# Kernel optimization log

Measured on AMD Instinct MI355X. Metric: run time of the kernel, lower is better.

The kernel has to match this reference:

```python
import jax, jax.numpy as jnp
import numpy as np

DIM = 512
HEADS = 8
DIM_HEAD = 64
INNER = HEADS * DIM_HEAD
SCALE = DIM_HEAD ** -0.5
EPS = 1e-5


def setup_inputs() -> dict:
    key = jax.random.key(0)
    ks = jax.random.split(key, 7)
    B, N = 8, 1024
    x = jax.random.normal(ks[0], (B, N, DIM), dtype=jnp.float32)
    ORquery = jax.random.normal(ks[1], (B, N, DIM), dtype=jnp.float32)
    alpha = jax.random.uniform(ks[2], (B, N, N), dtype=jnp.float32)
    # learned params (Linear layers without bias; stored as [in, out])
    w_qkv = jax.random.normal(ks[3], (DIM, INNER * 3), dtype=jnp.float32) * (DIM ** -0.5)
    w_orq = jax.random.normal(ks[4], (DIM, INNER), dtype=jnp.float32) * (DIM ** -0.5)
    w_out = jax.random.normal(ks[5], (INNER, DIM), dtype=jnp.float32) * (INNER ** -0.5)
    ln_w = jnp.ones((DIM,), dtype=jnp.float32)
    ln_b = jnp.zeros((DIM,), dtype=jnp.float32)
    return {"x": x, "ORquery": ORquery, "alpha": alpha, "ln_w": ln_w,
            "ln_b": ln_b, "w_qkv": w_qkv, "w_orq": w_orq, "w_out": w_out}


def _layernorm(x, w, b):
    mu = jnp.mean(x, axis=-1, keepdims=True)
    var = jnp.mean(jnp.square(x - mu), axis=-1, keepdims=True)
    return (x - mu) * jax.lax.rsqrt(var + EPS) * w + b


def _split_heads(t):  # [B, N, H*D] -> [B, H, N, D]
    B, N, _ = t.shape
    return t.reshape(B, N, HEADS, DIM_HEAD).transpose(0, 2, 1, 3)


def _merge_heads(t):  # [B, H, N, D] -> [B, N, H*D]
    B, H, N, D = t.shape
    return t.transpose(0, 2, 1, 3).reshape(B, N, H * D)


def reference(x, ORquery, alpha, ln_w, ln_b, w_qkv, w_orq, w_out):
    xn = _layernorm(x, ln_w, ln_b)
    qkv = xn @ w_qkv  # [B, N, 3*INNER]
    q, k, v = jnp.split(qkv, 3, axis=-1)
    q, k, v = _split_heads(q), _split_heads(k), _split_heads(v)

    # standard attention pass
    dots = jnp.einsum('bhid,bhjd->bhij', q, k) * SCALE
    attn = jax.nn.softmax(dots, axis=-1)
    out = _merge_heads(jnp.einsum('bhij,bhjd->bhid', attn, v))

    # OR-query pass: shared K/V, diagonal logits zeroed, (1-alpha^T) rescale
    orq = _split_heads(_layernorm(ORquery, ln_w, ln_b) @ w_orq)
    ordots = jnp.einsum('bhid,bhjd->bhij', orq, k) * SCALE
    N = ordots.shape[-1]
    eye = jnp.eye(N, dtype=bool)
    ordots = jnp.where(eye, 0.0, ordots)
    ordots = ordots * (1.0 - alpha.transpose(0, 2, 1)[:, None, :, :])
    orattn = jax.nn.softmax(ordots, axis=-1)
    orout = _merge_heads(jnp.einsum('bhij,bhjd->bhid', orattn, v))

    return (out @ w_out, orout @ w_out)
```

## Files before the change

kernel.cpp:

```cpp
#include <hip/hip_runtime.h>
#include <hip/hip_fp16.h>
#include <cstdint>
#include <cstddef>

typedef unsigned short u16;
typedef unsigned int u32;
typedef __attribute__((ext_vector_type(8))) short short8;
typedef __attribute__((ext_vector_type(4))) float f32x4;

static __device__ __forceinline__ u16 f2bf(float x) {
    u32 u = __builtin_bit_cast(u32, x);
    u += 0x7FFFu + ((u >> 16) & 1u);
    return (u16)(u >> 16);
}

static __device__ __forceinline__ void gload16(const void* g, void* l) {
    __builtin_amdgcn_global_load_lds(
        (const __attribute__((address_space(1))) u32*)g,
        (__attribute__((address_space(3))) u32*)l, 16, 0, 0);
}

#define SW(row, cb) (((row) * 64) + ((((cb) ^ ((row) & 7))) * 8))

#define C_L2E 0.18033688011112042f

static __device__ __forceinline__ void wtrans_body(
    const float* __restrict__ src, u16* __restrict__ dst, int R, int C,
    int bx, int by, float t[32][33])
{
    int c0 = bx * 32, r0 = by * 32;
    int tx = threadIdx.x & 31, ty = threadIdx.x >> 5;
    #pragma unroll
    for (int rr = 0; rr < 32; rr += 8)
        t[ty + rr][tx] = src[(size_t)(r0 + ty + rr) * C + c0 + tx];
    __syncthreads();
    #pragma unroll
    for (int rr = 0; rr < 32; rr += 8)
        dst[(size_t)(c0 + ty + rr) * R + r0 + tx] = f2bf(t[tx][ty + rr]);
}

__global__ __launch_bounds__(256) void prep_kernel(
    const float* __restrict__ x, const float* __restrict__ orqy,
    const float* __restrict__ alpha,
    const float* __restrict__ lw, const float* __restrict__ lb,
    const float* __restrict__ w_qkv, const float* __restrict__ w_orq,
    const float* __restrict__ w_out,
    u16* __restrict__ xn, u16* __restrict__ orqn,
    u16* __restrict__ wqkvT, u16* __restrict__ worqT, u16* __restrict__ woutT,
    u16* __restrict__ ascT)
{
    __shared__ float t[32][33];
    int id = blockIdx.x;
    if (id < 768) {
        wtrans_body(w_qkv, wqkvT, 512, 1536, id % 48, id / 48, t);
    } else if (id < 1024) {
        int r = id - 768;
        wtrans_body(w_orq, worqT, 512, 512, r & 15, r >> 4, t);
    } else if (id < 1280) {
        int r = id - 1024;
        wtrans_body(w_out, woutT, 512, 512, r & 15, r >> 4, t);
    } else if (id < 9472) {
        int r = id - 1280;
        int bx = r & 31, by = (r >> 5) & 31, b = r >> 10;
        int i0 = by * 32, j0 = bx * 32;
        int tx = threadIdx.x & 31, ty = threadIdx.x >> 5;
        const float* ab = alpha + ((size_t)b << 20);
        u16* atb = ascT + ((size_t)b << 20);
        #pragma unroll
        for (int rr = 0; rr < 32; rr += 8)
            t[ty + rr][tx] = ab[(size_t)(j0 + ty + rr) * 1024 + i0 + tx];
        __syncthreads();
        #pragma unroll
        for (int rr = 0; rr < 32; rr += 8) {
            float v = C_L2E * (1.0f - t[tx][ty + rr]);
            __half hv = __float2half_rn(v);
            atb[(size_t)(i0 + ty + rr) * 1024 + j0 + tx] = __builtin_bit_cast(u16, hv);
        }
    } else {
        int row = (id - 9472) * 4 + (threadIdx.x >> 6);
        const float* src;
        u16* dst;
        if (row < 8192) { src = x + (size_t)row * 512; dst = xn + (size_t)row * 512; }
        else { src = orqy + (size_t)(row - 8192) * 512; dst = orqn + (size_t)(row - 8192) * 512; }
        int lane = threadIdx.x & 63;
        float4 a = *(const float4*)(src + lane * 8);
        float4 b = *(const float4*)(src + lane * 8 + 4);
        float s = a.x + a.y + a.z + a.w + b.x + b.y + b.z + b.w;
        float q = a.x*a.x + a.y*a.y + a.z*a.z + a.w*a.w
                + b.x*b.x + b.y*b.y + b.z*b.z + b.w*b.w;
        #pragma unroll
        for (int off = 32; off >= 1; off >>= 1) {
            s += __shfl_xor(s, off);
            q += __shfl_xor(q, off);
        }
        float mu = s * (1.0f / 512.0f);
        float var = q * (1.0f / 512.0f) - mu * mu;
        float rs = 1.0f / sqrtf(var + 1e-5f);
        float4 w0 = *(const float4*)(lw + lane * 8);
        float4 w1 = *(const float4*)(lw + lane * 8 + 4);
        float4 b0 = *(const float4*)(lb + lane * 8);
        float4 b1 = *(const float4*)(lb + lane * 8 + 4);
        union { u16 h[8]; uint4 v; } ou;
        ou.h[0] = f2bf((a.x - mu) * rs * w0.x + b0.x);
        ou.h[1] = f2bf((a.y - mu) * rs * w0.y + b0.y);
        ou.h[2] = f2bf((a.z - mu) * rs * w0.z + b0.z);
        ou.h[3] = f2bf((a.w - mu) * rs * w0.w + b0.w);
        ou.h[4] = f2bf((b.x - mu) * rs * w1.x + b1.x);
        ou.h[5] = f2bf((b.y - mu) * rs * w1.y + b1.y);
        ou.h[6] = f2bf((b.z - mu) * rs * w1.z + b1.z);
        ou.h[7] = f2bf((b.w - mu) * rs * w1.w + b1.w);
        *(uint4*)(dst + lane * 8) = ou.v;
    }
}

__global__ __launch_bounds__(256) void gemm_kernel(
    const u16* __restrict__ A_, const u16* __restrict__ Bt_,
    const u16* __restrict__ A2, const u16* __restrict__ Bt2,
    int N, int K, int mode,
    u16* __restrict__ oq, u16* __restrict__ ok, u16* __restrict__ ov,
    u16* __restrict__ oq2, float* __restrict__ of)
{
    __shared__ u16 As[8192];
    __shared__ u16 Bs[8192];
    int bx = blockIdx.x;
    const u16* A = A_;
    const u16* Bt = Bt_;
    bool orqblk = false;
    if (mode == 3 && bx >= 12) { A = A2; Bt = Bt2; orqblk = true; bx -= 12; }
    int m0 = blockIdx.y * 128, n0 = bx * 128;
    int tid = threadIdx.x;
    int w = tid >> 6, lane = tid & 63;
    int lo = lane & 15, hi = lane >> 4;
    int wm = (w >> 1) * 64, wn = (w & 1) * 64;

    int sr0 = tid >> 2, sr1 = sr0 + 64;
    int sc0 = ((tid & 3) ^ ((sr0 >> 1) & 3)) * 8;
    int sc1 = ((tid & 3) ^ ((sr1 >> 1) & 3)) * 8;
    const u16* aS0 = A + (size_t)(m0 + sr0) * K + sc0;
    const u16* aS1 = A + (size_t)(m0 + sr1) * K + sc1;
    const u16* bS0 = Bt + (size_t)(n0 + sr0) * K + sc0;
    const u16* bS1 = Bt + (size_t)(n0 + sr1) * K + sc1;
    int d0 = w * 512, d1 = 2048 + w * 512;

    int aoff[4], boff[4];
    #pragma unroll
    for (int f = 0; f < 4; ++f) {
        int ra = wm + f * 16 + lo, rb = wn + f * 16 + lo;
        aoff[f] = ra * 32 + ((hi ^ ((ra >> 1) & 3)) * 8);
        boff[f] = rb * 32 + ((hi ^ ((rb >> 1) & 3)) * 8);
    }

    f32x4 acc[4][4] = {};
    int nk = K >> 5;
    gload16(aS0, &As[d0]);
    gload16(aS1, &As[d1]);
    gload16(bS0, &Bs[d0]);
    gload16(bS1, &Bs[d1]);
    __syncthreads();
    for (int kt = 0; kt < nk; ++kt) {
        int cur = (kt & 1) << 12;
        if (kt + 1 < nk) {
            int ko = (kt + 1) * 32;
            int nxt = ((kt + 1) & 1) << 12;
            gload16(aS0 + ko, &As[nxt + d0]);
            gload16(aS1 + ko, &As[nxt + d1]);
            gload16(bS0 + ko, &Bs[nxt + d0]);
            gload16(bS1 + ko, &Bs[nxt + d1]);
        }
        short8 af[4], bfr[4];
        #pragma unroll
        for (int mf = 0; mf < 4; ++mf) af[mf] = *(const short8*)&As[cur + aoff[mf]];
        #pragma unroll
        for (int nf = 0; nf < 4; ++nf) bfr[nf] = *(const short8*)&Bs[cur + boff[nf]];
        #pragma unroll
        for (int mf = 0; mf < 4; ++mf)
            #pragma unroll
            for (int nf = 0; nf < 4; ++nf)
                acc[mf][nf] = __builtin_amdgcn_mfma_f32_16x16x32_bf16(af[mf], bfr[nf], acc[mf][nf], 0, 0, 0);
        __syncthreads();
    }
    #pragma unroll
    for (int mf = 0; mf < 4; ++mf) {
        #pragma unroll
        for (int nf = 0; nf < 4; ++nf) {
            #pragma unroll
            for (int r = 0; r < 4; ++r) {
                int row = m0 + wm + mf * 16 + hi * 4 + r;
                int col = n0 + wn + nf * 16 + lo;
                float val = acc[mf][nf][r];
                if (mode == 2) {
                    of[(size_t)row * N + col] = val;
                } else {
                    int bb = row >> 10, i = row & 1023;
                    int h = (col >> 6) & 7;
                    int d = col & 63;
                    if (orqblk) {
                        oq2[(((size_t)bb * 8 + h) * 1024 + i) * 64 + d] = f2bf(val);
                    } else {
                        int which = col >> 9;
                        if (which == 0) val *= C_L2E;
                        u16 bv = f2bf(val);
                        if (which == 2) {
                            ov[(((size_t)bb * 8 + h) * 64 + d) * 1024 + i] = bv;
                        } else {
                            size_t idx = (((size_t)bb * 8 + h) * 1024 + i) * 64 + d;
                            (which == 0 ? oq : ok)[idx] = bv;
                        }
                    }
                }
            }
        }
    }
}

__global__ __launch_bounds__(512) void attn_fused_kernel(
    const u16* __restrict__ Q, const u16* __restrict__ OQ,
    const u16* __restrict__ Kk, const u16* __restrict__ Vt,
    const u16* __restrict__ asc,
    u16* __restrict__ outS, u16* __restrict__ outO)
{
    __shared__ u16 Kbuf[2][8192];
    __shared__ u16 Vbuf[2][8192];
    __shared__ u16 Ps[8192];

    int id = blockIdx.x;
    int swz = (id & 7) * 64 + (id >> 3);
    int bh = swz >> 3, it = swz & 7;
    int b = bh >> 3, h = bh & 7;
    int i0 = it * 128;
    int tid = threadIdx.x;
    int w = tid >> 6, lane = tid & 63;
    int lo = lane & 15, hi = lane >> 4;

    const u16* Qb = Q + ((size_t)bh * 1024 + i0) * 64;
    const u16* Ob = OQ + ((size_t)bh * 1024 + i0) * 64;
    const u16* Kb = Kk + (size_t)bh * 1024 * 64;
    const u16* Vb = Vt + (size_t)bh * 64 * 1024;

    int sxc = ((lane & 7) ^ (lane >> 3)) * 8;
    int krow0 = w * 16 + (lane >> 3);
    const u16* kS = Kb + (size_t)krow0 * 64 + sxc;
    int vrow = w * 8 + (lane >> 3);
    int sxv = ((lane & 7) ^ (vrow & 7)) * 8;
    const u16* vS = Vb + (size_t)vrow * 1024 + sxv;
    int kd = w * 1024;
    int vd = w * 512;

    const u16* AbL = asc + ((size_t)b << 20) + ((size_t)(i0 + w * 16 + hi * 4) << 10) + lo;

    int qrow = w * 16 + lo;
    short8 qS0 = *(const short8*)&Qb[qrow * 64 + hi * 8];
    short8 qS1 = *(const short8*)&Qb[qrow * 64 + 32 + hi * 8];
    short8 qO0 = *(const short8*)&Ob[qrow * 64 + hi * 8];
    short8 qO1 = *(const short8*)&Ob[qrow * 64 + 32 + hi * 8];

    int jtd = it * 2 + (w >> 2);

    gload16(kS, &Kbuf[0][kd]);
    gload16(kS + 512, &Kbuf[0][kd + 512]);
    gload16(vS, &Vbuf[0][vd]);
    gload16(vS + 64, &Vbuf[0][vd + 4096]);
    __syncthreads();

    f32x4 oS[4] = {}, oO[4] = {};
    float mS[4], lS[4], mO[4], lO[4];
    #pragma unroll
    for (int r = 0; r < 4; ++r) { mS[r] = -1e30f; lS[r] = 0.f; mO[r] = -1e30f; lO[r] = 0.f; }

    for (int jt = 0; jt < 8; ++jt) {
        int j0 = jt * 128;
        int c = jt & 1;

        u16 a_[32];
        #pragma unroll
        for (int sub = 0; sub < 2; ++sub)
            #pragma unroll
            for (int jf = 0; jf < 4; ++jf)
                #pragma unroll
                for (int r = 0; r < 4; ++r)
                    a_[sub * 16 + jf * 4 + r] = AbL[(size_t)(r << 10) + j0 + sub * 64 + jf * 16];

        if (jt < 7) {
            int jn = j0 + 128;
            gload16(kS + (size_t)jn * 64, &Kbuf[c ^ 1][kd]);
            gload16(kS + (size_t)(jn + 8) * 64, &Kbuf[c ^ 1][kd + 512]);
            gload16(vS + jn, &Vbuf[c ^ 1][vd]);
            gload16(vS + jn + 64, &Vbuf[c ^ 1][vd + 4096]);
        }

        #pragma unroll
        for (int sub = 0; sub < 2; ++sub) {
            const u16* Kc = &Kbuf[c][sub * 4096];
            const u16* Vc = &Vbuf[c][sub * 4096];
            const u16* al = &a_[sub * 16];

            f32x4 s[4];
            #pragma unroll
            for (int jf = 0; jf < 4; ++jf) {
                short8 kf0 = *(const short8*)&Kc[SW(jf * 16 + lo, hi)];
                short8 kf1 = *(const short8*)&Kc[SW(jf * 16 + lo, 4 + hi)];
                f32x4 z = {};
                z = __builtin_amdgcn_mfma_f32_16x16x32_bf16(qS0, kf0, z, 0, 0, 0);
                z = __builtin_amdgcn_mfma_f32_16x16x32_bf16(qS1, kf1, z, 0, 0, 0);
                s[jf] = z;
            }
            {
                float mx4[4];
                #pragma unroll
                for (int r = 0; r < 4; ++r)
                    mx4[r] = fmaxf(fmaxf(s[0][r], s[1][r]), fmaxf(s[2][r], s[3][r]));
                float need = fmaxf(fmaxf(mx4[0] - mS[0], mx4[1] - mS[1]),
                                   fmaxf(mx4[2] - mS[2], mx4[3] - mS[3]));
                if (!__all(need <= 8.0f)) {
                    #pragma unroll
                    for (int r = 0; r < 4; ++r) {
                        float mx = mx4[r];
                        #pragma unroll
                        for (int msk = 8; msk >= 1; msk >>= 1) mx = fmaxf(mx, __shfl_xor(mx, msk));
                        float mn = fmaxf(mS[r], mx);
                        float scl = __builtin_amdgcn_exp2f(mS[r] - mn);
                        mS[r] = mn;
                        lS[r] *= scl;
                        #pragma unroll
                        for (int df = 0; df < 4; ++df) oS[df][r] *= scl;
                    }
                }
                #pragma unroll
                for (int r = 0; r < 4; ++r)
                    #pragma unroll
                    for (int jf = 0; jf < 4; ++jf) {
                        float p = __builtin_amdgcn_exp2f(s[jf][r] - mS[r]);
                        s[jf][r] = p;
                        lS[r] += p;
                    }
            }
            #pragma unroll
            for (int jf = 0; jf < 4; ++jf)
                #pragma unroll
                for (int r = 0; r < 4; r += 2) {
                    int p0 = hi * 4 + r, p1 = p0 + 1;
                    u32 pk;
                    asm("v_cvt_pk_bf16_f32 %0, %1, %2" : "=v"(pk) : "v"(s[jf][r]), "v"(s[jf][r + 1]));
                    Ps[w * 1024 + p0 * 64 + ((jf * 16 + lo) ^ ((p0 & 7) * 8))] = (u16)pk;
                    Ps[w * 1024 + p1 * 64 + ((jf * 16 + lo) ^ ((p1 & 7) * 8))] = (u16)(pk >> 16);
                }
            {
                short8 pa0 = *(const short8*)&Ps[w * 1024 + SW(lo, hi)];
                short8 pa1 = *(const short8*)&Ps[w * 1024 + SW(lo, 4 + hi)];
                #pragma unroll
                for (int df = 0; df < 4; ++df) {
                    short8 v0 = *(const short8*)&Vc[SW(df * 16 + lo, hi)];
                    short8 v1 = *(const short8*)&Vc[SW(df * 16 + lo, 4 + hi)];
                    oS[df] = __builtin_amdgcn_mfma_f32_16x16x32_bf16(pa0, v0, oS[df], 0, 0, 0);
                    oS[df] = __builtin_amdgcn_mfma_f32_16x16x32_bf16(pa1, v1, oS[df], 0, 0, 0);
                }
            }

            #pragma unroll
            for (int jf = 0; jf < 4; ++jf) {
                short8 kf0 = *(const short8*)&Kc[SW(jf * 16 + lo, hi)];
                short8 kf1 = *(const short8*)&Kc[SW(jf * 16 + lo, 4 + hi)];
                f32x4 z = {};
                z = __builtin_amdgcn_mfma_f32_16x16x32_bf16(qO0, kf0, z, 0, 0, 0);
                z = __builtin_amdgcn_mfma_f32_16x16x32_bf16(qO1, kf1, z, 0, 0, 0);
                s[jf] = z;
            }
            #pragma unroll
            for (int jf = 0; jf < 4; ++jf)
                #pragma unroll
                for (int r = 0; r < 4; ++r) {
                    __half hv = __builtin_bit_cast(__half, al[jf * 4 + r]);
                    s[jf][r] *= __half2float(hv);
                }
            if (jt * 2 + sub == jtd) {
                #pragma unroll
                for (int jf = 0; jf < 4; ++jf)
                    #pragma unroll
                    for (int r = 0; r < 4; ++r)
                        s[jf][r] = ((jf == (w & 3)) && (hi * 4 + r == lo)) ? 0.0f : s[jf][r];
            }
            {
                float mx4[4];
                #pragma unroll
                for (int r = 0; r < 4; ++r)
                    mx4[r] = fmaxf(fmaxf(s[0][r], s[1][r]), fmaxf(s[2][r], s[3][r]));
                float need = fmaxf(fmaxf(mx4[0] - mO[0], mx4[1] - mO[1]),
                                   fmaxf(mx4[2] - mO[2], mx4[3] - mO[3]));
                if (!__all(need <= 8.0f)) {
                    #pragma unroll
                    for (int r = 0; r < 4; ++r) {
                        float mx = mx4[r];
                        #pragma unroll
                        for (int msk = 8; msk >= 1; msk >>= 1) mx = fmaxf(mx, __shfl_xor(mx, msk));
                        float mn = fmaxf(mO[r], mx);
                        float scl = __builtin_amdgcn_exp2f(mO[r] - mn);
                        mO[r] = mn;
                        lO[r] *= scl;
                        #pragma unroll
                        for (int df = 0; df < 4; ++df) oO[df][r] *= scl;
                    }
                }
                #pragma unroll
                for (int r = 0; r < 4; ++r)
                    #pragma unroll
                    for (int jf = 0; jf < 4; ++jf) {
                        float p = __builtin_amdgcn_exp2f(s[jf][r] - mO[r]);
                        s[jf][r] = p;
                        lO[r] += p;
                    }
            }
            #pragma unroll
            for (int jf = 0; jf < 4; ++jf)
                #pragma unroll
                for (int r = 0; r < 4; r += 2) {
                    int p0 = hi * 4 + r, p1 = p0 + 1;
                    u32 pk;
                    asm("v_cvt_pk_bf16_f32 %0, %1, %2" : "=v"(pk) : "v"(s[jf][r]), "v"(s[jf][r + 1]));
                    Ps[w * 1024 + p0 * 64 + ((jf * 16 + lo) ^ ((p0 & 7) * 8))] = (u16)pk;
                    Ps[w * 1024 + p1 * 64 + ((jf * 16 + lo) ^ ((p1 & 7) * 8))] = (u16)(pk >> 16);
                }
            {
                short8 pa0 = *(const short8*)&Ps[w * 1024 + SW(lo, hi)];
                short8 pa1 = *(const short8*)&Ps[w * 1024 + SW(lo, 4 + hi)];
                #pragma unroll
                for (int df = 0; df < 4; ++df) {
                    short8 v0 = *(const short8*)&Vc[SW(df * 16 + lo, hi)];
                    short8 v1 = *(const short8*)&Vc[SW(df * 16 + lo, 4 + hi)];
                    oO[df] = __builtin_amdgcn_mfma_f32_16x16x32_bf16(pa0, v0, oO[df], 0, 0, 0);
                    oO[df] = __builtin_amdgcn_mfma_f32_16x16x32_bf16(pa1, v1, oO[df], 0, 0, 0);
                }
            }
        }

        __syncthreads();
    }

    #pragma unroll
    for (int r = 0; r < 4; ++r) {
        float a = lS[r], c2 = lO[r];
        #pragma unroll
        for (int msk = 8; msk >= 1; msk >>= 1) {
            a += __shfl_xor(a, msk);
            c2 += __shfl_xor(c2, msk);
        }
        lS[r] = 1.0f / a;
        lO[r] = 1.0f / c2;
    }
    size_t obase = ((size_t)b * 1024 + i0 + w * 16 + hi * 4) * 512 + h * 64 + lo;
    #pragma unroll
    for (int df = 0; df < 4; ++df)
        #pragma unroll
        for (int r = 0; r < 4; ++r) {
            outS[obase + (size_t)r * 512 + df * 16] = f2bf(oS[df][r] * lS[r]);
            outO[obase + (size_t)r * 512 + df * 16] = f2bf(oO[df][r] * lO[r]);
        }
}

extern "C" void kernel_launch(void* const* d_in, const int* in_sizes, int n_in,
                              void* d_out, int out_size, void* d_ws, size_t ws_size,
                              hipStream_t stream)
{
    const float* x     = (const float*)d_in[0];
    const float* orqy  = (const float*)d_in[1];
    const float* alpha = (const float*)d_in[2];
    const float* ln_w  = (const float*)d_in[3];
    const float* ln_b  = (const float*)d_in[4];
    const float* w_qkv = (const float*)d_in[5];
    const float* w_orq = (const float*)d_in[6];
    const float* w_out = (const float*)d_in[7];
    float* outp = (float*)d_out;

    char* base = (char*)d_ws;
    size_t off = 0;
    auto alloc = [&](size_t bytes) -> char* {
        char* r = base + off;
        off += (bytes + 255) & ~(size_t)255;
        return r;
    };
    const size_t RC = 8192ull * 512 * 2;
    u16* xn       = (u16*)alloc(RC);
    u16* orqn     = (u16*)alloc(RC);
    u16* qb       = (u16*)alloc(RC);
    u16* kb       = (u16*)alloc(RC);
    u16* vb       = (u16*)alloc(RC);
    u16* orqb     = (u16*)alloc(RC);
    u16* attout   = (u16*)alloc(RC);
    u16* orattout = (u16*)alloc(RC);
    u16* wqkvT    = (u16*)alloc(1536ull * 512 * 2);
    u16* worqT    = (u16*)alloc(512ull * 512 * 2);
    u16* woutT    = (u16*)alloc(512ull * 512 * 2);
    u16* ascT     = (u16*)alloc(8ull * 1024 * 1024 * 2);

    prep_kernel<<<13568, 256, 0, stream>>>(x, orqy, alpha, ln_w, ln_b,
                                           w_qkv, w_orq, w_out,
                                           xn, orqn, wqkvT, worqT, woutT, ascT);
    gemm_kernel<<<dim3(16, 64), 256, 0, stream>>>(xn, wqkvT, orqn, worqT,
                                                  1536, 512, 3,
                                                  qb, kb, vb, orqb, nullptr);
    attn_fused_kernel<<<dim3(512), 512, 0, stream>>>(qb, orqb, kb, vb, ascT, attout, orattout);
    gemm_kernel<<<dim3(4, 128), 256, 0, stream>>>(attout, woutT, nullptr, nullptr,
                                                  512, 512, 2,
                                                  nullptr, nullptr, nullptr, nullptr, outp);
}
```

Baseline: 163.1 us.

## Overlap alpha and w_out transposes with GEMM/attention and enlarge GEMM tiles

After: 166.0 us. No clear change (+1.8%).

```diff
diff --git a/kernel.cpp b/kernel.cpp
--- a/kernel.cpp
+++ b/kernel.cpp
@@ -29,7 +29,7 @@
     int bx, int by, float t[32][33])
 {
     int c0 = bx * 32, r0 = by * 32;
-    int tx = threadIdx.x & 31, ty = threadIdx.x >> 5;
+    int tx = threadIdx.x & 31, ty = (threadIdx.x & 255) >> 5;
     #pragma unroll
     for (int rr = 0; rr < 32; rr += 8)
         t[ty + rr][tx] = src[(size_t)(r0 + ty + rr) * C + c0 + tx];
@@ -41,13 +41,10 @@
 
 __global__ __launch_bounds__(256) void prep_kernel(
     const float* __restrict__ x, const float* __restrict__ orqy,
-    const float* __restrict__ alpha,
     const float* __restrict__ lw, const float* __restrict__ lb,
     const float* __restrict__ w_qkv, const float* __restrict__ w_orq,
-    const float* __restrict__ w_out,
     u16* __restrict__ xn, u16* __restrict__ orqn,
-    u16* __restrict__ wqkvT, u16* __restrict__ worqT, u16* __restrict__ woutT,
-    u16* __restrict__ ascT)
+    u16* __restrict__ wqkvT, u16* __restrict__ worqT)
 {
     __shared__ float t[32][33];
     int id = blockIdx.x;
@@ -56,28 +53,8 @@
     } else if (id < 1024) {
         int r = id - 768;
         wtrans_body(w_orq, worqT, 512, 512, r & 15, r >> 4, t);
-    } else if (id < 1280) {
-        int r = id - 1024;
-        wtrans_body(w_out, woutT, 512, 512, r & 15, r >> 4, t);
-    } else if (id < 9472) {
-        int r = id - 1280;
-        int bx = r & 31, by = (r >> 5) & 31, b = r >> 10;
-        int i0 = by * 32, j0 = bx * 32;
-        int tx = threadIdx.x & 31, ty = threadIdx.x >> 5;
-        const float* ab = alpha + ((size_t)b << 20);
-        u16* atb = ascT + ((size_t)b << 20);
-        #pragma unroll
-        for (int rr = 0; rr < 32; rr += 8)
-            t[ty + rr][tx] = ab[(size_t)(j0 + ty + rr) * 1024 + i0 + tx];
-        __syncthreads();
-        #pragma unroll
-        for (int rr = 0; rr < 32; rr += 8) {
-            float v = C_L2E * (1.0f - t[tx][ty + rr]);
-            __half hv = __float2half_rn(v);
-            atb[(size_t)(i0 + ty + rr) * 1024 + j0 + tx] = __builtin_bit_cast(u16, hv);
-        }
     } else {
-        int row = (id - 9472) * 4 + (threadIdx.x >> 6);
+        int row = (id - 1024) * 4 + (threadIdx.x >> 6);
         const float* src;
         u16* dst;
         if (row < 8192) { src = x + (size_t)row * 512; dst = xn + (size_t)row * 512; }
@@ -113,34 +90,64 @@
     }
 }
 
-__global__ __launch_bounds__(256) void gemm_kernel(
+__global__ __launch_bounds__(512) void gemm_kernel(
     const u16* __restrict__ A_, const u16* __restrict__ Bt_,
     const u16* __restrict__ A2, const u16* __restrict__ Bt2,
+    const float* __restrict__ alpha, u16* __restrict__ ascT,
     int N, int K, int mode,
     u16* __restrict__ oq, u16* __restrict__ ok, u16* __restrict__ ov,
     u16* __restrict__ oq2, float* __restrict__ of)
 {
-    __shared__ u16 As[8192];
+    __shared__ u16 As[16384];
     __shared__ u16 Bs[8192];
+    int tid = threadIdx.x;
+
+    if (mode == 3 && blockIdx.y >= 32) {
+        float (*t)[32][33] = (float(*)[32][33])As;
+        int aid = blockIdx.x + (blockIdx.y - 32) * 16;
+        int sub = tid >> 8;
+        int t2 = tid & 255;
+        int tx = t2 & 31, ty = t2 >> 5;
+        for (int it2 = 0; it2 < 16; ++it2) {
+            int g = aid * 32 + it2 * 2 + sub;
+            int b = g >> 10, rr_ = g & 1023;
+            int i0 = (rr_ >> 5) * 32, j0 = (rr_ & 31) * 32;
+            const float* ab = alpha + ((size_t)b << 20);
+            u16* atb = ascT + ((size_t)b << 20);
+            #pragma unroll
+            for (int rr = 0; rr < 32; rr += 8)
+                t[sub][ty + rr][tx] = ab[(size_t)(j0 + ty + rr) * 1024 + i0 + tx];
+            __syncthreads();
+            #pragma unroll
+            for (int rr = 0; rr < 32; rr += 8) {
+                float v = C_L2E * (1.0f - t[sub][tx][ty + rr]);
+                __half hv = __float2half_rn(v);
+                atb[(size_t)(i0 + ty + rr) * 1024 + j0 + tx] = __builtin_bit_cast(u16, hv);
+            }
+            __syncthreads();
+        }
+        return;
+    }
+
     int bx = blockIdx.x;
     const u16* A = A_;
     const u16* Bt = Bt_;
     bool orqblk = false;
     if (mode == 3 && bx >= 12) { A = A2; Bt = Bt2; orqblk = true; bx -= 12; }
-    int m0 = blockIdx.y * 128, n0 = bx * 128;
-    int tid = threadIdx.x;
+    int m0 = blockIdx.y * 256, n0 = bx * 128;
     int w = tid >> 6, lane = tid & 63;
     int lo = lane & 15, hi = lane >> 4;
     int wm = (w >> 1) * 64, wn = (w & 1) * 64;
 
-    int sr0 = tid >> 2, sr1 = sr0 + 64;
-    int sc0 = ((tid & 3) ^ ((sr0 >> 1) & 3)) * 8;
-    int sc1 = ((tid & 3) ^ ((sr1 >> 1) & 3)) * 8;
-    const u16* aS0 = A + (size_t)(m0 + sr0) * K + sc0;
-    const u16* aS1 = A + (size_t)(m0 + sr1) * K + sc1;
-    const u16* bS0 = Bt + (size_t)(n0 + sr0) * K + sc0;
-    const u16* bS1 = Bt + (size_t)(n0 + sr1) * K + sc1;
-    int d0 = w * 512, d1 = 2048 + w * 512;
+    int arow0 = w * 32 + (lane >> 2);
+    int brow  = w * 16 + (lane >> 2);
+    int acb0 = ((lane & 3) ^ ((arow0 >> 1) & 3)) * 8;
+    int acb1 = ((lane & 3) ^ (((arow0 + 16) >> 1) & 3)) * 8;
+    int bcb  = ((lane & 3) ^ ((brow >> 1) & 3)) * 8;
+    const u16* aS0 = A + (size_t)(m0 + arow0) * K + acb0;
+    const u16* aS1 = A + (size_t)(m0 + arow0 + 16) * K + acb1;
+    const u16* bS0 = Bt + (size_t)(n0 + brow) * K + bcb;
+    int dA0 = w * 1024, dA1 = w * 1024 + 512, dB = w * 512;
 
     int aoff[4], boff[4];
     #pragma unroll
@@ -152,26 +159,26 @@
 
     f32x4 acc[4][4] = {};
     int nk = K >> 5;
-    gload16(aS0, &As[d0]);
-    gload16(aS1, &As[d1]);
-    gload16(bS0, &Bs[d0]);
-    gload16(bS1, &Bs[d1]);
+    gload16(aS0, &As[dA0]);
+    gload16(aS1, &As[dA1]);
+    gload16(bS0, &Bs[dB]);
     __syncthreads();
     for (int kt = 0; kt < nk; ++kt) {
-        int cur = (kt & 1) << 12;
+        int curA = (kt & 1) << 13;
+        int curB = (kt & 1) << 12;
         if (kt + 1 < nk) {
             int ko = (kt + 1) * 32;
-            int nxt = ((kt + 1) & 1) << 12;
-            gload16(aS0 + ko, &As[nxt + d0]);
-            gload16(aS1 + ko, &As[nxt + d1]);
-            gload16(bS0 + ko, &Bs[nxt + d0]);
-            gload16(bS1 + ko, &Bs[nxt + d1]);
+            int nxA = ((kt + 1) & 1) << 13;
+            int nxB = ((kt + 1) & 1) << 12;
+            gload16(aS0 + ko, &As[nxA + dA0]);
+            gload16(aS1 + ko, &As[nxA + dA1]);
+            gload16(bS0 + ko, &Bs[nxB + dB]);
         }
         short8 af[4], bfr[4];
         #pragma unroll
-        for (int mf = 0; mf < 4; ++mf) af[mf] = *(const short8*)&As[cur + aoff[mf]];
-        #pragma unroll
-        for (int nf = 0; nf < 4; ++nf) bfr[nf] = *(const short8*)&Bs[cur + boff[nf]];
+        for (int mf = 0; mf < 4; ++mf) af[mf] = *(const short8*)&As[curA + aoff[mf]];
+        #pragma unroll
+        for (int nf = 0; nf < 4; ++nf) bfr[nf] = *(const short8*)&Bs[curB + boff[nf]];
         #pragma unroll
         for (int mf = 0; mf < 4; ++mf)
             #pragma unroll
@@ -217,18 +224,36 @@
     const u16* __restrict__ Q, const u16* __restrict__ OQ,
     const u16* __restrict__ Kk, const u16* __restrict__ Vt,
     const u16* __restrict__ asc,
+    const float* __restrict__ w_out, u16* __restrict__ woutT,
     u16* __restrict__ outS, u16* __restrict__ outO)
 {
     __shared__ u16 Kbuf[2][8192];
     __shared__ u16 Vbuf[2][8192];
     __shared__ u16 Ps[8192];
 
+    int tid = threadIdx.x;
+    if (blockIdx.x >= 512) {
+        float (*tw)[32][33] = (float(*)[32][33])Kbuf;
+        int sub = tid >> 8;
+        int g = (blockIdx.x - 512) * 2 + sub;
+        int c0 = (g & 15) * 32, r0 = (g >> 4) * 32;
+        int t2 = tid & 255;
+        int tx = t2 & 31, ty = t2 >> 5;
+        #pragma unroll
+        for (int rr = 0; rr < 32; rr += 8)
+            tw[sub][ty + rr][tx] = w_out[(size_t)(r0 + ty + rr) * 512 + c0 + tx];
+        __syncthreads();
+        #pragma unroll
+        for (int rr = 0; rr < 32; rr += 8)
+            woutT[(size_t)(c0 + ty + rr) * 512 + r0 + tx] = f2bf(tw[sub][tx][ty + rr]);
+        return;
+    }
+
     int id = blockIdx.x;
     int swz = (id & 7) * 64 + (id >> 3);
     int bh = swz >> 3, it = swz & 7;
     int b = bh >> 3, h = bh & 7;
     int i0 = it * 128;
-    int tid = threadIdx.x;
     int w = tid >> 6, lane = tid & 63;
     int lo = lane & 15, hi = lane >> 4;
 
@@ -491,14 +516,16 @@
     u16* woutT    = (u16*)alloc(512ull * 512 * 2);
     u16* ascT     = (u16*)alloc(8ull * 1024 * 1024 * 2);
 
-    prep_kernel<<<13568, 256, 0, stream>>>(x, orqy, alpha, ln_w, ln_b,
-                                           w_qkv, w_orq, w_out,
-                                           xn, orqn, wqkvT, worqT, woutT, ascT);
-    gemm_kernel<<<dim3(16, 64), 256, 0, stream>>>(xn, wqkvT, orqn, worqT,
+    prep_kernel<<<5120, 256, 0, stream>>>(x, orqy, ln_w, ln_b, w_qkv, w_orq,
+                                          xn, orqn, wqkvT, worqT);
+    gemm_kernel<<<dim3(16, 48), 512, 0, stream>>>(xn, wqkvT, orqn, worqT,
+                                                  alpha, ascT,
                                                   1536, 512, 3,
                                                   qb, kb, vb, orqb, nullptr);
-    attn_fused_kernel<<<dim3(512), 512, 0, stream>>>(qb, orqb, kb, vb, ascT, attout, orattout);
-    gemm_kernel<<<dim3(4, 128), 256, 0, stream>>>(attout, woutT, nullptr, nullptr,
-                                                  512, 512, 2,
-                                                  nullptr, nullptr, nullptr, nullptr, outp);
-}
+    attn_fused_kernel<<<dim3(640), 512, 0, stream>>>(qb, orqb, kb, vb, ascT,
+                                                     w_out, woutT, attout, orattout);
+    gemm_kernel<<<dim3(4, 64), 512, 0, stream>>>(attout, woutT, nullptr, nullptr,
+                                                 nullptr, nullptr,
+                                                 512, 512, 2,
+                                                 nullptr, nullptr, nullptr, nullptr, outp);
+}
```
